# Kernel tuning notes

Measured on AMD Instinct MI355X. Metric: run time of the kernel, lower is better.

Reference implementation:

```python
import jax, jax.numpy as jnp
import numpy as np

NUM_TOKENS = 1024  # codebook size (n_embed)
CODE_DIM = 256     # embedding_dim
BETA = 0.25


def setup_inputs() -> dict:
    key = jax.random.key(0)
    k1, k2 = jax.random.split(key)
    z = jax.random.normal(k1, (64, 512, CODE_DIM), dtype=jnp.float32)
    weight = jax.random.normal(k2, (NUM_TOKENS, CODE_DIM), dtype=jnp.float32)
    return {"z": z, "weight": weight}


def reference(z, weight):
    # z: [B, T, D]; weight: [K, D]
    z_flat = z.reshape(-1, CODE_DIM)                       # [N, D]
    # squared euclidean distances: ||z||^2 + ||w||^2 - 2 z.w
    d = (jnp.sum(z_flat ** 2, axis=1, keepdims=True)
         + jnp.sum(weight ** 2, axis=1)
         - 2.0 * jnp.matmul(z_flat, weight.T))             # [N, K]
    min_encoding_indices = jnp.argmin(d, axis=1)           # [N]
    z_q = weight[min_encoding_indices].reshape(z.shape)    # gather

    # perplexity from mean one-hot usage (avoid materializing one-hot via bincount)
    counts = jnp.bincount(min_encoding_indices, length=NUM_TOKENS)
    e_mean = counts.astype(z.dtype) / z_flat.shape[0]
    perplexity = jnp.exp(-jnp.sum(e_mean * jnp.log(e_mean + 1e-10)))

    # commitment loss (codebook is EMA-updated, so z_q is detached)
    loss = BETA * jnp.mean((jax.lax.stop_gradient(z_q) - z) ** 2)
    # straight-through estimator
    z_q_st = z + jax.lax.stop_gradient(z_q - z)
    return (loss, z_q_st, min_encoding_indices, perplexity)
```

## Files before the change

kernel.cpp:

```cpp
#include <hip/hip_runtime.h>

#define N_TOKENS 32768
#define K_CODES  1024
#define DIM      256
#define BETA     0.25f

typedef unsigned long long u64;
typedef _Float16 half8 __attribute__((ext_vector_type(8)));
typedef float floatx4 __attribute__((ext_vector_type(4)));

__global__ void init_kernel(const float* __restrict__ w, float* __restrict__ wn,
                            int* __restrict__ counts, u64* __restrict__ keys,
                            _Float16* __restrict__ whiG, _Float16* __restrict__ wloG) {
    int k = blockIdx.x;
    int lane = threadIdx.x;
    float4 v = *(const float4*)(w + (size_t)k * DIM + lane * 4);
    float vals[4] = {v.x, v.y, v.z, v.w};
    float s = 0.f;
    #pragma unroll
    for (int e = 0; e < 4; e++) {
        s += vals[e] * vals[e];
        _Float16 h = (_Float16)vals[e];
        whiG[k * DIM + lane * 4 + e] = h;
        wloG[k * DIM + lane * 4 + e] = (_Float16)(vals[e] - (float)h);
    }
    #pragma unroll
    for (int off = 32; off; off >>= 1) s += __shfl_down(s, off);
    if (lane == 0) { wn[k] = s; counts[k] = 0; }
    if (lane < 32) keys[k * 32 + lane] = ~0ull;
}

__global__ __launch_bounds__(256, 2) void argmin_kernel(
    const float* __restrict__ z, const _Float16* __restrict__ whiG,
    const _Float16* __restrict__ wloG, const float* __restrict__ wn,
    u64* __restrict__ keys)
{
    constexpr int ZS = 40;
    __shared__ _Float16 whi[256 * ZS], wlo[256 * ZS];

    const int tid  = threadIdx.x;
    const int lane = tid & 63;
    const int wid  = tid >> 6;
    const int wm   = wid >> 1;
    const int wq   = wid & 1;
    const int t_   = blockIdx.x & 255;
    const int q    = blockIdx.x >> 8;
    const int tok0  = t_ * 128;
    const int kbase = q * 256;

    float wnr[8];
    #pragma unroll
    for (int j = 0; j < 8; j++)
        wnr[j] = wn[kbase + wq * 128 + j * 16 + (lane & 15)];

    floatx4 acc[4][8];
    #pragma unroll
    for (int i = 0; i < 4; i++)
        #pragma unroll
        for (int j = 0; j < 8; j++)
            acc[i][j] = (floatx4){0.f, 0.f, 0.f, 0.f};

    const int r0 = tid >> 2;
    const int g0 = tid & 3;
    const int kg = lane >> 4;

    const float* zA = z + (size_t)(tok0 + wm * 64 + (lane & 15)) * DIM + kg * 8;

    for (int dt = 0; dt < 8; ++dt) {
        const int d0 = dt * 32;
        __syncthreads();

        #pragma unroll
        for (int s = 0; s < 4; s++) {
            int t = r0 + s * 64;
            size_t goff = (size_t)(kbase + t) * DIM + d0 + g0 * 8;
            *(half8*)&whi[t * ZS + g0 * 8] = *(const half8*)&whiG[goff];
            *(half8*)&wlo[t * ZS + g0 * 8] = *(const half8*)&wloG[goff];
        }
        __syncthreads();

        half8 ah[4], al[4];
        #pragma unroll
        for (int i = 0; i < 4; i++) {
            const float* p = zA + (size_t)i * 16 * DIM + d0;
            float4 a = *(const float4*)p;
            float4 b = *(const float4*)(p + 4);
            float vals[8] = {a.x, a.y, a.z, a.w, b.x, b.y, b.z, b.w};
            #pragma unroll
            for (int e = 0; e < 8; e++) {
                _Float16 h = (_Float16)vals[e];
                ah[i][e] = h;
                al[i][e] = (_Float16)(vals[e] - (float)h);
            }
        }

        const int koff = kg * 8;
        __builtin_amdgcn_s_setprio(1);
        #pragma unroll
        for (int j = 0; j < 8; j++) {
            int off = (wq * 128 + j * 16 + (lane & 15)) * ZS + koff;
            half8 bh = *(const half8*)&whi[off];
            half8 bl = *(const half8*)&wlo[off];
            #pragma unroll
            for (int i = 0; i < 4; i++) {
                acc[i][j] = __builtin_amdgcn_mfma_f32_16x16x32_f16(ah[i], bh, acc[i][j], 0, 0, 0);
                acc[i][j] = __builtin_amdgcn_mfma_f32_16x16x32_f16(ah[i], bl, acc[i][j], 0, 0, 0);
                acc[i][j] = __builtin_amdgcn_mfma_f32_16x16x32_f16(al[i], bh, acc[i][j], 0, 0, 0);
            }
        }
        __builtin_amdgcn_s_setprio(0);
    }

    #pragma unroll
    for (int i = 0; i < 4; i++) {
        #pragma unroll
        for (int r = 0; r < 4; r++) {
            float bv = 3.4e38f; int bi = 0;
            #pragma unroll
            for (int j = 0; j < 8; j++) {
                int cl = wq * 128 + j * 16 + (lane & 15);
                float dist = wnr[j] - 2.0f * acc[i][j][r];
                if (dist < bv) { bv = dist; bi = kbase + cl; }
            }
            unsigned uu = __float_as_uint(bv);
            unsigned ss = (uu & 0x80000000u) ? ~uu : (uu | 0x80000000u);
            u64 key = ((u64)ss << 32) | (unsigned)bi;
            #pragma unroll
            for (int m = 1; m < 16; m <<= 1) {
                u64 o = __shfl_xor(key, m);
                if (o < key) key = o;
            }
            if ((lane & 15) == 0) {
                int token = tok0 + wm * 64 + i * 16 + (lane >> 4) * 4 + r;
                atomicMin(&keys[token], key);
            }
        }
    }
}

__global__ void gather_loss_kernel(const float* __restrict__ z,
                                   const float* __restrict__ w,
                                   const u64* __restrict__ keys,
                                   float* __restrict__ zq_out,
                                   float* __restrict__ idxf,
                                   int* __restrict__ counts,
                                   float* __restrict__ partials)
{
    __shared__ float red[4];
    int tid = threadIdx.x;
    int lane = tid & 63;
    int wid = blockIdx.x * 4 + (tid >> 6);
    float s = 0.0f;
    #pragma unroll
    for (int it = 0; it < 4; it++) {
        int tok = wid + it * 8192;
        u64 key = 0;
        if (lane == 0) key = keys[tok];
        key = __shfl(key, 0);
        int k = (int)(key & (u64)(K_CODES - 1));
        float4 wv = *(const float4*)(w + (size_t)k * DIM + lane * 4);
        float4 zv = *(const float4*)(z + (size_t)tok * DIM + lane * 4);
        *(float4*)(zq_out + (size_t)tok * DIM + lane * 4) = wv;
        float dx = wv.x - zv.x, dy = wv.y - zv.y, dz = wv.z - zv.z, dw = wv.w - zv.w;
        s += dx * dx + dy * dy + dz * dz + dw * dw;
        if (lane == 0) {
            idxf[tok] = (float)k;
            atomicAdd(&counts[k], 1);
        }
    }
    #pragma unroll
    for (int off = 32; off; off >>= 1) s += __shfl_down(s, off);
    if (lane == 0) red[tid >> 6] = s;
    __syncthreads();
    if (tid == 0)
        partials[blockIdx.x] = red[0] + red[1] + red[2] + red[3];
}

__global__ void finalize_kernel(const int* __restrict__ counts,
                                const float* __restrict__ partials,
                                float* __restrict__ loss_out,
                                float* __restrict__ ppl_out)
{
    __shared__ float redE[16], redL[16];
    int tid = threadIdx.x;
    float e = (float)counts[tid] * (1.0f / (float)N_TOKENS);
    float t = -e * logf(e + 1e-10f);
    float p = partials[tid] + partials[tid + 1024];
    #pragma unroll
    for (int off = 32; off; off >>= 1) {
        t += __shfl_down(t, off);
        p += __shfl_down(p, off);
    }
    if ((tid & 63) == 0) { redE[tid >> 6] = t; redL[tid >> 6] = p; }
    __syncthreads();
    if (tid == 0) {
        float se = 0.0f, sl = 0.0f;
        #pragma unroll
        for (int i = 0; i < 16; i++) { se += redE[i]; sl += redL[i]; }
        *ppl_out = expf(se);
        *loss_out = BETA * sl / (float)((size_t)N_TOKENS * DIM);
    }
}

extern "C" void kernel_launch(void* const* d_in, const int* in_sizes, int n_in,
                              void* d_out, int out_size, void* d_ws, size_t ws_size,
                              hipStream_t stream) {
    const float* z = (const float*)d_in[0];
    const float* w = (const float*)d_in[1];
    float* out = (float*)d_out;

    float* loss_out = out;
    float* zq_out   = out + 1;
    float* idxf     = out + 1 + (size_t)N_TOKENS * DIM;
    float* ppl_out  = out + (out_size - 1);

    float* wn       = (float*)d_ws;
    int*   counts   = (int*)d_ws + 1024;
    float* partials = (float*)d_ws + 2048;
    u64*   keys     = (u64*)((char*)d_ws + 16384);
    _Float16* whiG  = (_Float16*)((char*)d_ws + 16384 + (size_t)N_TOKENS * 8);
    _Float16* wloG  = whiG + (size_t)K_CODES * DIM;

    init_kernel<<<K_CODES, 64, 0, stream>>>(w, wn, counts, keys, whiG, wloG);
    argmin_kernel<<<4 * 256, 256, 0, stream>>>(z, whiG, wloG, wn, keys);
    gather_loss_kernel<<<2048, 256, 0, stream>>>(z, w, keys, zq_out, idxf, counts, partials);
    finalize_kernel<<<1, 1024, 0, stream>>>(counts, partials, loss_out, ppl_out);
}
```

Baseline: 169.8 us.

## Double-buffer codebook tiles with register prefetch, XOR swizzle, and halve code tile

Restructures the argmin GEMM loop so each block prefetches the next 32-wide slice of codebook and z into registers while computing on the current LDS buffer, using two LDS buffers and a single barrier per step. The LDS layout changes from a padded stride to an XOR-swizzled 64-byte row to avoid bank conflicts. The code tile per block is halved to 128 codes, which doubles the grid and cuts accumulator registers. This lets more waves fit per CU, but z is now re-read and re-split into fp16 parts twice as often across blocks, and more atomicMin operations are issued.

```diff
diff --git a/kernel.cpp b/kernel.cpp
--- a/kernel.cpp
+++ b/kernel.cpp
@@ -35,8 +35,7 @@
     const _Float16* __restrict__ wloG, const float* __restrict__ wn,
     u64* __restrict__ keys)
 {
-    constexpr int ZS = 40;
-    __shared__ _Float16 whi[256 * ZS], wlo[256 * ZS];
+    __shared__ __attribute__((aligned(16))) char wb[2][16384];
 
     const int tid  = threadIdx.x;
     const int lane = tid & 63;
@@ -44,72 +43,112 @@
     const int wm   = wid >> 1;
     const int wq   = wid & 1;
     const int t_   = blockIdx.x & 255;
-    const int q    = blockIdx.x >> 8;
+    const int q8   = blockIdx.x >> 8;
     const int tok0  = t_ * 128;
-    const int kbase = q * 256;
-
-    float wnr[8];
-    #pragma unroll
-    for (int j = 0; j < 8; j++)
-        wnr[j] = wn[kbase + wq * 128 + j * 16 + (lane & 15)];
-
-    floatx4 acc[4][8];
+    const int kbase = q8 * 128;
+
+    float wnr[4];
+    #pragma unroll
+    for (int j = 0; j < 4; j++)
+        wnr[j] = wn[kbase + wq * 64 + j * 16 + (lane & 15)];
+
+    floatx4 acc[4][4];
     #pragma unroll
     for (int i = 0; i < 4; i++)
         #pragma unroll
-        for (int j = 0; j < 8; j++)
+        for (int j = 0; j < 4; j++)
             acc[i][j] = (floatx4){0.f, 0.f, 0.f, 0.f};
 
-    const int r0 = tid >> 2;
-    const int g0 = tid & 3;
+    const int r0w = tid >> 1;
+    const int g0w = (tid & 1) * 16;
+    const int swzw = (r0w & 3) << 4;
+    const int wbyte0 = r0w * 64 + ((2 * g0w) ^ swzw);
+    const int wbyte1 = r0w * 64 + ((2 * g0w + 16) ^ swzw);
+    const _Float16* whg = whiG + (size_t)(kbase + r0w) * DIM + g0w;
+    const _Float16* wlg = wloG + (size_t)(kbase + r0w) * DIM + g0w;
+
     const int kg = lane >> 4;
+    const int rb = (wq * 64 + (lane & 15)) * 64 + ((kg * 16) ^ ((lane & 3) << 4));
 
     const float* zA = z + (size_t)(tok0 + wm * 64 + (lane & 15)) * DIM + kg * 8;
 
-    for (int dt = 0; dt < 8; ++dt) {
-        const int d0 = dt * 32;
-        __syncthreads();
-
-        #pragma unroll
-        for (int s = 0; s < 4; s++) {
-            int t = r0 + s * 64;
-            size_t goff = (size_t)(kbase + t) * DIM + d0 + g0 * 8;
-            *(half8*)&whi[t * ZS + g0 * 8] = *(const half8*)&whiG[goff];
-            *(half8*)&wlo[t * ZS + g0 * 8] = *(const half8*)&wloG[goff];
-        }
-        __syncthreads();
-
-        half8 ah[4], al[4];
-        #pragma unroll
-        for (int i = 0; i < 4; i++) {
-            const float* p = zA + (size_t)i * 16 * DIM + d0;
-            float4 a = *(const float4*)p;
-            float4 b = *(const float4*)(p + 4);
-            float vals[8] = {a.x, a.y, a.z, a.w, b.x, b.y, b.z, b.w};
-            #pragma unroll
-            for (int e = 0; e < 8; e++) {
-                _Float16 h = (_Float16)vals[e];
-                ah[i][e] = h;
-                al[i][e] = (_Float16)(vals[e] - (float)h);
-            }
-        }
-
-        const int koff = kg * 8;
-        __builtin_amdgcn_s_setprio(1);
-        #pragma unroll
-        for (int j = 0; j < 8; j++) {
-            int off = (wq * 128 + j * 16 + (lane & 15)) * ZS + koff;
-            half8 bh = *(const half8*)&whi[off];
-            half8 bl = *(const half8*)&wlo[off];
-            #pragma unroll
-            for (int i = 0; i < 4; i++) {
-                acc[i][j] = __builtin_amdgcn_mfma_f32_16x16x32_f16(ah[i], bh, acc[i][j], 0, 0, 0);
-                acc[i][j] = __builtin_amdgcn_mfma_f32_16x16x32_f16(ah[i], bl, acc[i][j], 0, 0, 0);
-                acc[i][j] = __builtin_amdgcn_mfma_f32_16x16x32_f16(al[i], bh, acc[i][j], 0, 0, 0);
-            }
-        }
-        __builtin_amdgcn_s_setprio(0);
-    }
+    float4 zrA[8], zrB[8];
+    half8 wha, whb, wla, wlb;
+
+#define LOADW(dtn) do { \
+    wha = *(const half8*)(whg + (dtn) * 32); \
+    whb = *(const half8*)(whg + (dtn) * 32 + 8); \
+    wla = *(const half8*)(wlg + (dtn) * 32); \
+    wlb = *(const half8*)(wlg + (dtn) * 32 + 8); \
+} while (0)
+
+#define WRITEW(b) do { \
+    *(half8*)&wb[b][wbyte0] = wha; \
+    *(half8*)&wb[b][wbyte1] = whb; \
+    *(half8*)&wb[b][8192 + wbyte0] = wla; \
+    *(half8*)&wb[b][8192 + wbyte1] = wlb; \
+} while (0)
+
+#define LOADA(dtn, zr) do { \
+    const float* p0 = zA + (dtn) * 32; \
+    zr[0] = *(const float4*)p0;                      zr[1] = *(const float4*)(p0 + 4); \
+    const float* p1 = zA + (size_t)16 * DIM + (dtn) * 32; \
+    zr[2] = *(const float4*)p1;                      zr[3] = *(const float4*)(p1 + 4); \
+    const float* p2 = zA + (size_t)32 * DIM + (dtn) * 32; \
+    zr[4] = *(const float4*)p2;                      zr[5] = *(const float4*)(p2 + 4); \
+    const float* p3 = zA + (size_t)48 * DIM + (dtn) * 32; \
+    zr[6] = *(const float4*)p3;                      zr[7] = *(const float4*)(p3 + 4); \
+} while (0)
+
+#define STEP(dt, cur, zc, zl) do { \
+    if ((dt) < 7) { LOADW((dt) + 1); LOADA((dt) + 1, zl); } \
+    half8 ah[4], al[4]; \
+    _Pragma("unroll") \
+    for (int i = 0; i < 4; i++) { \
+        float vals[8] = {zc[2*i].x, zc[2*i].y, zc[2*i].z, zc[2*i].w, \
+                         zc[2*i+1].x, zc[2*i+1].y, zc[2*i+1].z, zc[2*i+1].w}; \
+        _Pragma("unroll") \
+        for (int e = 0; e < 8; e++) { \
+            _Float16 h = (_Float16)vals[e]; \
+            ah[i][e] = h; \
+            al[i][e] = (_Float16)(vals[e] - (float)h); \
+        } \
+    } \
+    __builtin_amdgcn_s_setprio(1); \
+    _Pragma("unroll") \
+    for (int j = 0; j < 4; j++) { \
+        half8 bh = *(const half8*)&wb[cur][rb + j * 1024]; \
+        half8 bl = *(const half8*)&wb[cur][rb + j * 1024 + 8192]; \
+        _Pragma("unroll") \
+        for (int i = 0; i < 4; i++) { \
+            acc[i][j] = __builtin_amdgcn_mfma_f32_16x16x32_f16(ah[i], bh, acc[i][j], 0, 0, 0); \
+            acc[i][j] = __builtin_amdgcn_mfma_f32_16x16x32_f16(ah[i], bl, acc[i][j], 0, 0, 0); \
+            acc[i][j] = __builtin_amdgcn_mfma_f32_16x16x32_f16(al[i], bh, acc[i][j], 0, 0, 0); \
+        } \
+    } \
+    __builtin_amdgcn_s_setprio(0); \
+    if ((dt) < 7) WRITEW((cur) ^ 1); \
+    __syncthreads(); \
+} while (0)
+
+    LOADW(0);
+    LOADA(0, zrA);
+    WRITEW(0);
+    __syncthreads();
+
+    STEP(0, 0, zrA, zrB);
+    STEP(1, 1, zrB, zrA);
+    STEP(2, 0, zrA, zrB);
+    STEP(3, 1, zrB, zrA);
+    STEP(4, 0, zrA, zrB);
+    STEP(5, 1, zrB, zrA);
+    STEP(6, 0, zrA, zrB);
+    STEP(7, 1, zrB, zrA);
+
+#undef LOADW
+#undef WRITEW
+#undef LOADA
+#undef STEP
 
     #pragma unroll
     for (int i = 0; i < 4; i++) {
@@ -117,8 +156,8 @@
         for (int r = 0; r < 4; r++) {
             float bv = 3.4e38f; int bi = 0;
             #pragma unroll
-            for (int j = 0; j < 8; j++) {
-                int cl = wq * 128 + j * 16 + (lane & 15);
+            for (int j = 0; j < 4; j++) {
+                int cl = wq * 64 + j * 16 + (lane & 15);
                 float dist = wnr[j] - 2.0f * acc[i][j][r];
                 if (dist < bv) { bv = dist; bi = kbase + cl; }
             }
@@ -222,7 +261,7 @@
     _Float16* wloG  = whiG + (size_t)K_CODES * DIM;
 
     init_kernel<<<K_CODES, 64, 0, stream>>>(w, wn, counts, keys, whiG, wloG);
-    argmin_kernel<<<4 * 256, 256, 0, stream>>>(z, whiG, wloG, wn, keys);
+    argmin_kernel<<<8 * 256, 256, 0, stream>>>(z, whiG, wloG, wn, keys);
     gather_loss_kernel<<<2048, 256, 0, stream>>>(z, w, keys, zq_out, idxf, counts, partials);
     finalize_kernel<<<1, 1024, 0, stream>>>(counts, partials, loss_out, ppl_out);
 }
```

After: 203.3 us. 19.7% more time.
